# Performance work log

Measured on AMD Instinct MI355X. Metric: run time of the kernel, lower is better.

Reference implementation:

```python
import jax, jax.numpy as jnp
import numpy as np

N = 100000
E = 1600000
D = 128


def setup_inputs() -> dict:
    key = jax.random.key(0)
    k1, k2, k3 = jax.random.split(key, 3)
    indices = jax.random.randint(k1, (2, E), 0, N, dtype=jnp.int64)
    values = jax.random.normal(k2, (E,), dtype=jnp.float32)
    b = jax.random.normal(k3, (N, D), dtype=jnp.float32)
    return {"indices": indices, "values": values, "n": N, "b": b}


def reference(indices, values, n, b):
    # Sparse COO SpMM: out[r] = sum_{e: row[e]==r} values[e] * b[col[e]]
    row, col = indices[0], indices[1]
    contrib = values[:, None] * b[col]          # [E, D] gather-multiply
    out = jax.ops.segment_sum(contrib, row, num_segments=n)  # [N, D] scatter-add
    return out
```

## Files before the change

### kernel.cpp

```cpp
#include <hip/hip_runtime.h>
#include <hip/hip_fp16.h>


#define D_DIM 128
#define RPB 64
#define RPB_SHIFT 6
#define MAXB 2048
#define CAP_LDS 1408
#define EPT 6
#define EPT1 8
#define OVF_MAX 65536

typedef float fx4 __attribute__((ext_vector_type(4)));

__global__ __launch_bounds__(256) void convert_b_kernel(
        const float* __restrict__ b, __half* __restrict__ bh, int n8) {
    int i = blockIdx.x * blockDim.x + threadIdx.x;
    if (i >= n8) return;
    const float4* b4 = (const float4*)b;
    float4 a0 = b4[2 * i];
    float4 a1 = b4[2 * i + 1];
    union { __half2 h[4]; uint4 u; } pk;
    pk.h[0] = __floats2half2_rn(a0.x, a0.y);
    pk.h[1] = __floats2half2_rn(a0.z, a0.w);
    pk.h[2] = __floats2half2_rn(a1.x, a1.y);
    pk.h[3] = __floats2half2_rn(a1.z, a1.w);
    ((uint4*)bh)[i] = pk.u;
}

__global__ __launch_bounds__(1024) void phase1_partition(
        const int* __restrict__ rows,
        const int* __restrict__ cols,
        const float* __restrict__ vals,
        int* __restrict__ bucket_cnt,
        int2* __restrict__ packed,
        int* __restrict__ ovf_cnt,
        int* __restrict__ ovf_list,
        int E, int nb, int cap, int chunk) {
    __shared__ int hist[MAXB];
    int tid = threadIdx.x;
    int start = blockIdx.x * chunk;
    int end = start + chunk; if (end > E) end = E;

    for (int i = tid; i < nb; i += 1024) hist[i] = 0;
    __syncthreads();

    int rr[EPT1]; int cc[EPT1]; float vv[EPT1];
    int ne = 0;
    for (int e = start + tid; e < end; e += 1024) {
        int r = rows[e];
        if (ne < EPT1) { rr[ne] = r; cc[ne] = cols[e]; vv[ne] = vals[e]; }
        ++ne;
        atomicAdd(&hist[r >> RPB_SHIFT], 1);
    }
    __syncthreads();

    for (int bkt = tid; bkt < nb; bkt += 1024) {
        int c = hist[bkt];
        hist[bkt] = (c > 0) ? atomicAdd(&bucket_cnt[bkt], c) : 0;
    }
    __syncthreads();

    int j = 0;
    for (int e = start + tid; e < end; e += 1024, ++j) {
        int r, c; float v;
        if (j < EPT1) { r = rr[j]; c = cc[j]; v = vv[j]; }
        else          { r = rows[e]; c = cols[e]; v = vals[e]; }
        int bkt = r >> RPB_SHIFT;
        int local = atomicAdd(&hist[bkt], 1);
        if (local < cap) {
            int key = ((r & (RPB - 1)) << 17) | c;
            packed[(size_t)bkt * cap + local] = make_int2(key, __float_as_int(v));
        } else {
            int k = atomicAdd(ovf_cnt, 1);
            if (k < OVF_MAX) ovf_list[k] = e;
        }
    }
}

template <bool HALF>
__global__ __launch_bounds__(256) void phase2_sort_gather(
        const int* __restrict__ bucket_cnt,
        const int2* __restrict__ packed,
        const __half* __restrict__ bh,
        const float* __restrict__ b,
        float* __restrict__ out,
        int cap, int N) {
    __shared__ int2 sorted[CAP_LDS];
    __shared__ int hist[RPB];
    __shared__ int offs[RPB + 1];
    __shared__ int cursor[RPB];

    int bucket = blockIdx.x;
    int tid = threadIdx.x;

    int cnt = bucket_cnt[bucket];
    if (cnt > cap) cnt = cap;
    const int2* pk = packed + (size_t)bucket * cap;

    if (tid < RPB) hist[tid] = 0;
    __syncthreads();

    int2 ev[EPT];
    int  rl[EPT];
    int ne = 0;
    for (int i = tid; i < cnt; i += 256) {
        int2 e = pk[i];
        ev[ne] = e;
        rl[ne] = ((unsigned)e.x) >> 17;
        atomicAdd(&hist[rl[ne]], 1);
        ++ne;
    }
    __syncthreads();

    for (int d = 1; d < RPB; d <<= 1) {
        int t = (tid < RPB && tid >= d) ? hist[tid - d] : 0;
        __syncthreads();
        if (tid < RPB) hist[tid] += t;
        __syncthreads();
    }
    if (tid == 0) offs[0] = 0;
    if (tid < RPB) {
        offs[tid + 1] = hist[tid];
        cursor[tid] = (tid == 0) ? 0 : hist[tid - 1];
    }
    __syncthreads();

    for (int j = 0; j < ne; ++j) {
        int pos = atomicAdd(&cursor[rl[j]], 1);
        sorted[pos] = make_int2(ev[j].x & 0x1FFFF, ev[j].y);
    }
    __syncthreads();

    int g = tid >> 5;
    int glane = tid & 31;
    int r0 = bucket << RPB_SHIFT;
    for (int k = 0; k < 8; ++k) {
        int rr = g * 8 + k;
        int start = offs[rr];
        int num = offs[rr + 1] - start;
        float4 acc = make_float4(0.f, 0.f, 0.f, 0.f);
        for (int base = 0; base < num; base += 8) {
#pragma unroll
            for (int j = 0; j < 8; ++j) {
                int idx = base + j;
                int sidx = start + ((idx < num) ? idx : (num - 1));
                int2 e = sorted[sidx];
                float v = (idx < num) ? __int_as_float(e.y) : 0.f;
                if (HALF) {
                    uint2 hv = ((const uint2*)(bh + (size_t)e.x * D_DIM))[glane];
                    __half2* hp = (__half2*)&hv;
                    float2 f0 = __half22float2(hp[0]);
                    float2 f1 = __half22float2(hp[1]);
                    acc.x += v * f0.x;
                    acc.y += v * f0.y;
                    acc.z += v * f1.x;
                    acc.w += v * f1.y;
                } else {
                    float4 bv = ((const float4*)(b + (size_t)e.x * D_DIM))[glane];
                    acc.x += v * bv.x;
                    acc.y += v * bv.y;
                    acc.z += v * bv.z;
                    acc.w += v * bv.w;
                }
            }
        }
        int r = r0 + rr;
        if (r < N) {
            fx4 av = {acc.x, acc.y, acc.z, acc.w};
            __builtin_nontemporal_store(av, (fx4*)(out + (size_t)r * D_DIM) + glane);
        }
    }
}

__global__ void fixup_kernel(const int* __restrict__ ovf_cnt,
                             const int* __restrict__ ovf_list,
                             const int* __restrict__ rows,
                             const int* __restrict__ cols,
                             const float* __restrict__ vals,
                             const float* __restrict__ b,
                             float* __restrict__ out) {
    int items = *ovf_cnt;
    if (items > OVF_MAX) items = OVF_MAX;
    int gsz  = (gridDim.x * blockDim.x) >> 5;
    int gid  = (blockIdx.x * blockDim.x + threadIdx.x) >> 5;
    int lane = threadIdx.x & 31;
    for (int i = gid; i < items; i += gsz) {
        int e = ovf_list[i];
        int r = rows[e];
        int c = cols[e];
        float v = vals[e];
        float4 bv = ((const float4*)(b + (size_t)c * D_DIM))[lane];
        float* op = out + (size_t)r * D_DIM + (size_t)lane * 4;
        atomicAdd(op + 0, v * bv.x);
        atomicAdd(op + 1, v * bv.y);
        atomicAdd(op + 2, v * bv.z);
        atomicAdd(op + 3, v * bv.w);
    }
}

__global__ void spmm_atomic_kernel(const int* __restrict__ rows,
                                   const int* __restrict__ cols,
                                   const float* __restrict__ vals,
                                   const float* __restrict__ b,
                                   float* __restrict__ out, int E) {
    int t = blockIdx.x * blockDim.x + threadIdx.x;
    int e = t >> 5;
    if (e >= E) return;
    int lane = t & 31;
    int r = rows[e];
    int c = cols[e];
    float v = vals[e];
    float4 bv = ((const float4*)(b + (size_t)c * D_DIM))[lane];
    float* op = out + (size_t)r * D_DIM + (size_t)lane * 4;
    atomicAdd(op + 0, v * bv.x);
    atomicAdd(op + 1, v * bv.y);
    atomicAdd(op + 2, v * bv.z);
    atomicAdd(op + 3, v * bv.w);
}

extern "C" void kernel_launch(void* const* d_in, const int* in_sizes, int n_in,
                              void* d_out, int out_size, void* d_ws, size_t ws_size,
                              hipStream_t stream) {
    const int*   indices = (const int*)d_in[0];
    const float* vals    = (const float*)d_in[1];
    const float* b       = (const float*)d_in[3];
    float*       out     = (float*)d_out;

    int E = in_sizes[1];
    int N = out_size / D_DIM;
    const int* rows = indices;
    const int* cols = indices + E;

    int nb = (N + RPB - 1) >> RPB_SHIFT;
    int avg = (nb > 0) ? E / nb : 0;
    int cap = CAP_LDS;

    size_t fixed      = (size_t)nb * 4 + 4 + (size_t)OVF_MAX * 4;
    size_t bh_off     = (fixed + 255) & ~(size_t)255;
    size_t bh_bytes   = (size_t)N * D_DIM * 2;
    size_t packed_h   = (bh_off + bh_bytes + 255) & ~(size_t)255;
    size_t packed_f   = bh_off;
    size_t need_h     = packed_h + (size_t)nb * cap * 8;
    size_t need_f     = packed_f + (size_t)nb * cap * 8;

    bool okBase = (nb <= MAXB) && (N <= 131072) && (cap > avg + avg / 8);
    bool useHalf = okBase && (ws_size >= need_h);
    bool useF32  = okBase && !useHalf && (ws_size >= need_f);

    if (!useHalf && !useF32) {
        (void)hipMemsetAsync(d_out, 0, (size_t)out_size * sizeof(float), stream);
        long long total = (long long)E * 32;
        int blocks = (int)((total + 255) / 256);
        spmm_atomic_kernel<<<blocks, 256, 0, stream>>>(rows, cols, vals, b, out, E);
        return;
    }

    char* w = (char*)d_ws;
    int*    bucket_cnt = (int*)w;
    int*    ovf_cnt    = (int*)(w + (size_t)nb * 4);
    int*    ovf_list   = (int*)(w + (size_t)nb * 4 + 4);
    __half* bh         = (__half*)(w + bh_off);
    int2*   packed     = (int2*)(w + (useHalf ? packed_h : packed_f));

    (void)hipMemsetAsync(bucket_cnt, 0, (size_t)nb * 4 + 4, stream);

    if (useHalf) {
        int n8 = N * D_DIM / 8;
        convert_b_kernel<<<(n8 + 255) / 256, 256, 0, stream>>>(b, bh, n8);
    }

    const int P1_WGS = 256;
    int chunk = (E + P1_WGS - 1) / P1_WGS;
    phase1_partition<<<P1_WGS, 1024, 0, stream>>>(
        rows, cols, vals, bucket_cnt, packed, ovf_cnt, ovf_list, E, nb, cap, chunk);

    if (useHalf)
        phase2_sort_gather<true><<<nb, 256, 0, stream>>>(
            bucket_cnt, packed, bh, b, out, cap, N);
    else
        phase2_sort_gather<false><<<nb, 256, 0, stream>>>(
            bucket_cnt, packed, bh, b, out, cap, N);

    fixup_kernel<<<8, 256, 0, stream>>>(ovf_cnt, ovf_list, rows, cols, vals, b, out);
}
```

Baseline: 215.3 us.

## Fuse fp16 conversion into partition kernel, pad bucket counters, nontemporal loads

The separate kernel that converts b to fp16 is folded into the partition launch as extra workgroups, so conversion runs alongside partitioning and one launch is saved. Each global bucket counter is now spaced 16 ints apart to cut atomic contention from false sharing on the same cache line. The phase-2 reads of packed entries use nontemporal loads to avoid polluting the cache. The counter padding enlarges the workspace, and the conversion blocks compete with partition blocks for CUs.

```diff
diff --git a/kernel.cpp b/kernel.cpp
--- a/kernel.cpp
+++ b/kernel.cpp
@@ -12,23 +12,9 @@
 #define OVF_MAX 65536
 
 typedef float fx4 __attribute__((ext_vector_type(4)));
-
-__global__ __launch_bounds__(256) void convert_b_kernel(
-        const float* __restrict__ b, __half* __restrict__ bh, int n8) {
-    int i = blockIdx.x * blockDim.x + threadIdx.x;
-    if (i >= n8) return;
-    const float4* b4 = (const float4*)b;
-    float4 a0 = b4[2 * i];
-    float4 a1 = b4[2 * i + 1];
-    union { __half2 h[4]; uint4 u; } pk;
-    pk.h[0] = __floats2half2_rn(a0.x, a0.y);
-    pk.h[1] = __floats2half2_rn(a0.z, a0.w);
-    pk.h[2] = __floats2half2_rn(a1.x, a1.y);
-    pk.h[3] = __floats2half2_rn(a1.z, a1.w);
-    ((uint4*)bh)[i] = pk.u;
-}
-
-__global__ __launch_bounds__(1024) void phase1_partition(
+typedef int   ix2 __attribute__((ext_vector_type(2)));
+
+__global__ __launch_bounds__(1024) void phase1_fused(
         const int* __restrict__ rows,
         const int* __restrict__ cols,
         const float* __restrict__ vals,
@@ -36,9 +22,29 @@
         int2* __restrict__ packed,
         int* __restrict__ ovf_cnt,
         int* __restrict__ ovf_list,
-        int E, int nb, int cap, int chunk) {
+        int E, int nb, int cap, int chunk, int cs,
+        int nPart,
+        const float* __restrict__ b, __half* __restrict__ bh, int n8) {
     __shared__ int hist[MAXB];
     int tid = threadIdx.x;
+
+    if ((int)blockIdx.x >= nPart) {
+        int idx = ((int)blockIdx.x - nPart) * 1024 + tid;
+        int stride = ((int)gridDim.x - nPart) * 1024;
+        const float4* b4 = (const float4*)b;
+        for (int i = idx; i < n8; i += stride) {
+            float4 a0 = b4[2 * i];
+            float4 a1 = b4[2 * i + 1];
+            union { __half2 h[4]; uint4 u; } pk;
+            pk.h[0] = __floats2half2_rn(a0.x, a0.y);
+            pk.h[1] = __floats2half2_rn(a0.z, a0.w);
+            pk.h[2] = __floats2half2_rn(a1.x, a1.y);
+            pk.h[3] = __floats2half2_rn(a1.z, a1.w);
+            ((uint4*)bh)[i] = pk.u;
+        }
+        return;
+    }
+
     int start = blockIdx.x * chunk;
     int end = start + chunk; if (end > E) end = E;
 
@@ -57,7 +63,7 @@
 
     for (int bkt = tid; bkt < nb; bkt += 1024) {
         int c = hist[bkt];
-        hist[bkt] = (c > 0) ? atomicAdd(&bucket_cnt[bkt], c) : 0;
+        hist[bkt] = (c > 0) ? atomicAdd(&bucket_cnt[bkt << cs], c) : 0;
     }
     __syncthreads();
 
@@ -85,7 +91,7 @@
         const __half* __restrict__ bh,
         const float* __restrict__ b,
         float* __restrict__ out,
-        int cap, int N) {
+        int cap, int N, int cs) {
     __shared__ int2 sorted[CAP_LDS];
     __shared__ int hist[RPB];
     __shared__ int offs[RPB + 1];
@@ -94,9 +100,9 @@
     int bucket = blockIdx.x;
     int tid = threadIdx.x;
 
-    int cnt = bucket_cnt[bucket];
+    int cnt = bucket_cnt[bucket << cs];
     if (cnt > cap) cnt = cap;
-    const int2* pk = packed + (size_t)bucket * cap;
+    const ix2* pk = (const ix2*)(packed + (size_t)bucket * cap);
 
     if (tid < RPB) hist[tid] = 0;
     __syncthreads();
@@ -105,7 +111,8 @@
     int  rl[EPT];
     int ne = 0;
     for (int i = tid; i < cnt; i += 256) {
-        int2 e = pk[i];
+        ix2 ee = __builtin_nontemporal_load(&pk[i]);
+        int2 e = make_int2(ee.x, ee.y);
         ev[ne] = e;
         rl[ne] = ((unsigned)e.x) >> 17;
         atomicAdd(&hist[rl[ne]], 1);
@@ -236,17 +243,26 @@
     int avg = (nb > 0) ? E / nb : 0;
     int cap = CAP_LDS;
 
-    size_t fixed      = (size_t)nb * 4 + 4 + (size_t)OVF_MAX * 4;
-    size_t bh_off     = (fixed + 255) & ~(size_t)255;
-    size_t bh_bytes   = (size_t)N * D_DIM * 2;
-    size_t packed_h   = (bh_off + bh_bytes + 255) & ~(size_t)255;
-    size_t packed_f   = bh_off;
-    size_t need_h     = packed_h + (size_t)nb * cap * 8;
-    size_t need_f     = packed_f + (size_t)nb * cap * 8;
-
     bool okBase = (nb <= MAXB) && (N <= 131072) && (cap > avg + avg / 8);
-    bool useHalf = okBase && (ws_size >= need_h);
-    bool useF32  = okBase && !useHalf && (ws_size >= need_f);
+    int cs = 4;
+    bool useHalf = false, useF32 = false;
+    size_t cnt_bytes = 0, bh_off = 0, packed_off = 0;
+    size_t bh_bytes = (size_t)N * D_DIM * 2;
+
+    for (int attempt = 0; attempt < 2 && okBase; ++attempt) {
+        cnt_bytes = ((size_t)nb << cs) * 4;
+        size_t fixed = cnt_bytes + 4 + (size_t)OVF_MAX * 4;
+        size_t bho   = (fixed + 255) & ~(size_t)255;
+        size_t pk_h  = (bho + bh_bytes + 255) & ~(size_t)255;
+        size_t pk_f  = bho;
+        if (ws_size >= pk_h + (size_t)nb * cap * 8) {
+            useHalf = true; bh_off = bho; packed_off = pk_h; break;
+        }
+        if (ws_size >= pk_f + (size_t)nb * cap * 8) {
+            useF32 = true; bh_off = bho; packed_off = pk_f; break;
+        }
+        cs = 0;
+    }
 
     if (!useHalf && !useF32) {
         (void)hipMemsetAsync(d_out, 0, (size_t)out_size * sizeof(float), stream);
@@ -258,29 +274,28 @@
 
     char* w = (char*)d_ws;
     int*    bucket_cnt = (int*)w;
-    int*    ovf_cnt    = (int*)(w + (size_t)nb * 4);
-    int*    ovf_list   = (int*)(w + (size_t)nb * 4 + 4);
+    int*    ovf_cnt    = (int*)(w + cnt_bytes);
+    int*    ovf_list   = (int*)(w + cnt_bytes + 4);
     __half* bh         = (__half*)(w + bh_off);
-    int2*   packed     = (int2*)(w + (useHalf ? packed_h : packed_f));
-
-    (void)hipMemsetAsync(bucket_cnt, 0, (size_t)nb * 4 + 4, stream);
-
-    if (useHalf) {
-        int n8 = N * D_DIM / 8;
-        convert_b_kernel<<<(n8 + 255) / 256, 256, 0, stream>>>(b, bh, n8);
-    }
+    int2*   packed     = (int2*)(w + packed_off);
+
+    (void)hipMemsetAsync(bucket_cnt, 0, cnt_bytes + 4, stream);
 
     const int P1_WGS = 256;
     int chunk = (E + P1_WGS - 1) / P1_WGS;
-    phase1_partition<<<P1_WGS, 1024, 0, stream>>>(
-        rows, cols, vals, bucket_cnt, packed, ovf_cnt, ovf_list, E, nb, cap, chunk);
+    int n8 = N * D_DIM / 8;
+    int nConv = useHalf ? ((n8 + 1024 * 2 - 1) / (1024 * 2)) : 0;
+
+    phase1_fused<<<P1_WGS + nConv, 1024, 0, stream>>>(
+        rows, cols, vals, bucket_cnt, packed, ovf_cnt, ovf_list,
+        E, nb, cap, chunk, cs, P1_WGS, b, bh, n8);
 
     if (useHalf)
         phase2_sort_gather<true><<<nb, 256, 0, stream>>>(
-            bucket_cnt, packed, bh, b, out, cap, N);
+            bucket_cnt, packed, bh, b, out, cap, N, cs);
     else
         phase2_sort_gather<false><<<nb, 256, 0, stream>>>(
-            bucket_cnt, packed, bh, b, out, cap, N);
+            bucket_cnt, packed, bh, b, out, cap, N, cs);
 
     fixup_kernel<<<8, 256, 0, stream>>>(ovf_cnt, ovf_list, rows, cols, vals, b, out);
 }
```

New measurement: 227.1 us. 1.06x slower.

## Split feature dimension into column slices for phase2 gather with sliced half layout

Applied to the files above, without the earlier changes.

Converts b into a slice-major half layout in which each 16-column slice of all rows is stored contiguously. Phase 2 now launches one workgroup per (slice, bucket), with four lanes per row covering that slice, so each slice's gather working set (about 3.2 MB) is small enough to stay in cache. The cost is that every workgroup repeats the bucket load, histogram and LDS sort eight times, and each gathered row piece is only 32 bytes, which may lower memory efficiency.

```diff
diff --git a/kernel.cpp b/kernel.cpp
--- a/kernel.cpp
+++ b/kernel.cpp
@@ -10,22 +10,30 @@
 #define EPT 6
 #define EPT1 8
 #define OVF_MAX 65536
+#define NSLICE 8
+#define SLICE_COLS 16
 
 typedef float fx4 __attribute__((ext_vector_type(4)));
 
-__global__ __launch_bounds__(256) void convert_b_kernel(
-        const float* __restrict__ b, __half* __restrict__ bh, int n8) {
-    int i = blockIdx.x * blockDim.x + threadIdx.x;
-    if (i >= n8) return;
-    const float4* b4 = (const float4*)b;
-    float4 a0 = b4[2 * i];
-    float4 a1 = b4[2 * i + 1];
-    union { __half2 h[4]; uint4 u; } pk;
+__global__ __launch_bounds__(256) void convert_b_slice(
+        const float* __restrict__ b, __half* __restrict__ bh, int N) {
+    int i = blockIdx.x * 256 + threadIdx.x;
+    if (i >= N * NSLICE) return;
+    int row = i >> 3, slice = i & 7;
+    const float4* src = (const float4*)(b + (size_t)row * D_DIM + slice * SLICE_COLS);
+    float4 a0 = src[0], a1 = src[1], a2 = src[2], a3 = src[3];
+    union { __half2 h[8]; uint4 u[2]; } pk;
     pk.h[0] = __floats2half2_rn(a0.x, a0.y);
     pk.h[1] = __floats2half2_rn(a0.z, a0.w);
     pk.h[2] = __floats2half2_rn(a1.x, a1.y);
     pk.h[3] = __floats2half2_rn(a1.z, a1.w);
-    ((uint4*)bh)[i] = pk.u;
+    pk.h[4] = __floats2half2_rn(a2.x, a2.y);
+    pk.h[5] = __floats2half2_rn(a2.z, a2.w);
+    pk.h[6] = __floats2half2_rn(a3.x, a3.y);
+    pk.h[7] = __floats2half2_rn(a3.z, a3.w);
+    uint4* dst = (uint4*)(bh + (size_t)slice * N * SLICE_COLS + (size_t)row * SLICE_COLS);
+    dst[0] = pk.u[0];
+    dst[1] = pk.u[1];
 }
 
 __global__ __launch_bounds__(1024) void phase1_partition(
@@ -79,7 +87,7 @@
 }
 
 template <bool HALF>
-__global__ __launch_bounds__(256) void phase2_sort_gather(
+__global__ __launch_bounds__(256) void phase2_sliced(
         const int* __restrict__ bucket_cnt,
         const int2* __restrict__ packed,
         const __half* __restrict__ bh,
@@ -91,7 +99,8 @@
     __shared__ int offs[RPB + 1];
     __shared__ int cursor[RPB];
 
-    int bucket = blockIdx.x;
+    int bucket = blockIdx.y;
+    int slice  = blockIdx.x;
     int tid = threadIdx.x;
 
     int cnt = bucket_cnt[bucket];
@@ -132,44 +141,43 @@
     }
     __syncthreads();
 
-    int g = tid >> 5;
-    int glane = tid & 31;
-    int r0 = bucket << RPB_SHIFT;
-    for (int k = 0; k < 8; ++k) {
-        int rr = g * 8 + k;
-        int start = offs[rr];
-        int num = offs[rr + 1] - start;
-        float4 acc = make_float4(0.f, 0.f, 0.f, 0.f);
-        for (int base = 0; base < num; base += 8) {
+    int s = tid >> 2;
+    int lane4 = tid & 3;
+    const __half* bs = bh + (size_t)slice * N * SLICE_COLS;
+    int start = offs[s];
+    int num = offs[s + 1] - start;
+    float4 acc = make_float4(0.f, 0.f, 0.f, 0.f);
+    for (int base = 0; base < num; base += 8) {
 #pragma unroll
-            for (int j = 0; j < 8; ++j) {
-                int idx = base + j;
-                int sidx = start + ((idx < num) ? idx : (num - 1));
-                int2 e = sorted[sidx];
-                float v = (idx < num) ? __int_as_float(e.y) : 0.f;
-                if (HALF) {
-                    uint2 hv = ((const uint2*)(bh + (size_t)e.x * D_DIM))[glane];
-                    __half2* hp = (__half2*)&hv;
-                    float2 f0 = __half22float2(hp[0]);
-                    float2 f1 = __half22float2(hp[1]);
-                    acc.x += v * f0.x;
-                    acc.y += v * f0.y;
-                    acc.z += v * f1.x;
-                    acc.w += v * f1.y;
-                } else {
-                    float4 bv = ((const float4*)(b + (size_t)e.x * D_DIM))[glane];
-                    acc.x += v * bv.x;
-                    acc.y += v * bv.y;
-                    acc.z += v * bv.z;
-                    acc.w += v * bv.w;
-                }
+        for (int j = 0; j < 8; ++j) {
+            int idx = base + j;
+            int sidx = start + ((idx < num) ? idx : (num - 1));
+            int2 e = sorted[sidx];
+            float v = (idx < num) ? __int_as_float(e.y) : 0.f;
+            if (HALF) {
+                uint2 hv = ((const uint2*)(bs + (size_t)e.x * SLICE_COLS))[lane4];
+                __half2* hp = (__half2*)&hv;
+                float2 f0 = __half22float2(hp[0]);
+                float2 f1 = __half22float2(hp[1]);
+                acc.x += v * f0.x;
+                acc.y += v * f0.y;
+                acc.z += v * f1.x;
+                acc.w += v * f1.y;
+            } else {
+                float4 bv = ((const float4*)(b + (size_t)e.x * D_DIM
+                                             + slice * SLICE_COLS))[lane4];
+                acc.x += v * bv.x;
+                acc.y += v * bv.y;
+                acc.z += v * bv.z;
+                acc.w += v * bv.w;
             }
         }
-        int r = r0 + rr;
-        if (r < N) {
-            fx4 av = {acc.x, acc.y, acc.z, acc.w};
-            __builtin_nontemporal_store(av, (fx4*)(out + (size_t)r * D_DIM) + glane);
-        }
+    }
+    int r = (bucket << RPB_SHIFT) + s;
+    if (r < N) {
+        fx4 av = {acc.x, acc.y, acc.z, acc.w};
+        __builtin_nontemporal_store(av,
+            (fx4*)(out + (size_t)r * D_DIM + slice * SLICE_COLS) + lane4);
     }
 }
 
@@ -266,8 +274,8 @@
     (void)hipMemsetAsync(bucket_cnt, 0, (size_t)nb * 4 + 4, stream);
 
     if (useHalf) {
-        int n8 = N * D_DIM / 8;
-        convert_b_kernel<<<(n8 + 255) / 256, 256, 0, stream>>>(b, bh, n8);
+        int items = N * NSLICE;
+        convert_b_slice<<<(items + 255) / 256, 256, 0, stream>>>(b, bh, N);
     }
 
     const int P1_WGS = 256;
@@ -275,11 +283,12 @@
     phase1_partition<<<P1_WGS, 1024, 0, stream>>>(
         rows, cols, vals, bucket_cnt, packed, ovf_cnt, ovf_list, E, nb, cap, chunk);
 
+    dim3 g2(NSLICE, nb);
     if (useHalf)
-        phase2_sort_gather<true><<<nb, 256, 0, stream>>>(
+        phase2_sliced<true><<<g2, 256, 0, stream>>>(
             bucket_cnt, packed, bh, b, out, cap, N);
     else
-        phase2_sort_gather<false><<<nb, 256, 0, stream>>>(
+        phase2_sliced<false><<<g2, 256, 0, stream>>>(
             bucket_cnt, packed, bh, b, out, cap, N);
 
     fixup_kernel<<<8, 256, 0, stream>>>(ovf_cnt, ovf_list, rows, cols, vals, b, out);
```

Result: slower. 255.4 us (+18.6%).

## Add per-row fixed-capacity bucketing path with one-row-per-32-lane-group gather

Applied to the files above, without the earlier changes.

Adds a new path that scatters COO entries into fixed-capacity per-row slots via a global atomic counter per row. A second kernel then has each 32-lane group sum one output row from the fp16 copy of b and write it directly. This replaces the 64-row bucket partition plus LDS sort stage, removing the sort and the atomic output accumulation. In exchange it performs a global atomic per edge, leaves slots unused for rows with fewer entries, and sends entries past capacity (up to 40) to the overflow fixup. The path is taken whenever the workspace can hold at least 28 slots per row.

```diff
diff --git a/kernel.cpp b/kernel.cpp
--- a/kernel.cpp
+++ b/kernel.cpp
@@ -10,6 +10,8 @@
 #define EPT 6
 #define EPT1 8
 #define OVF_MAX 65536
+#define CAPR_MIN 28
+#define CAPR_MAX 40
 
 typedef float fx4 __attribute__((ext_vector_type(4)));
 
@@ -27,6 +29,80 @@
     pk.h[3] = __floats2half2_rn(a1.z, a1.w);
     ((uint4*)bh)[i] = pk.u;
 }
+
+
+__global__ __launch_bounds__(256) void phase1_rows(
+        const int* __restrict__ rows,
+        const int* __restrict__ cols,
+        const float* __restrict__ vals,
+        int* __restrict__ row_cnt,
+        int2* __restrict__ packed,
+        int* __restrict__ ovf_cnt,
+        int* __restrict__ ovf_list,
+        int E, int capr) {
+    int idx = blockIdx.x * 256 + threadIdx.x;
+    int stride = gridDim.x * 256;
+    for (int e = idx; e < E; e += stride) {
+        int r = rows[e];
+        int c = cols[e];
+        float v = vals[e];
+        int local = atomicAdd(&row_cnt[r], 1);
+        if (local < capr) {
+            packed[(size_t)r * capr + local] = make_int2(c, __float_as_int(v));
+        } else {
+            int k = atomicAdd(ovf_cnt, 1);
+            if (k < OVF_MAX) ovf_list[k] = e;
+        }
+    }
+}
+
+template <bool HALF>
+__global__ __launch_bounds__(256) void phase2_rows(
+        const int* __restrict__ row_cnt,
+        const int2* __restrict__ packed,
+        const __half* __restrict__ bh,
+        const float* __restrict__ b,
+        float* __restrict__ out,
+        int capr, int N) {
+    int g = threadIdx.x >> 5;
+    int glane = threadIdx.x & 31;
+    int r = blockIdx.x * 8 + g;
+    if (r >= N) return;
+
+    int cnt = row_cnt[r];
+    if (cnt > capr) cnt = capr;
+    const int2* pk = packed + (size_t)r * capr;
+
+    float4 acc = make_float4(0.f, 0.f, 0.f, 0.f);
+    for (int base = 0; base < cnt; base += 8) {
+#pragma unroll
+        for (int j = 0; j < 8; ++j) {
+            int idx = base + j;
+            int sidx = (idx < cnt) ? idx : (cnt - 1);
+            int2 e = pk[sidx];
+            float v = (idx < cnt) ? __int_as_float(e.y) : 0.f;
+            if (HALF) {
+                uint2 hv = ((const uint2*)(bh + (size_t)e.x * D_DIM))[glane];
+                __half2* hp = (__half2*)&hv;
+                float2 f0 = __half22float2(hp[0]);
+                float2 f1 = __half22float2(hp[1]);
+                acc.x += v * f0.x;
+                acc.y += v * f0.y;
+                acc.z += v * f1.x;
+                acc.w += v * f1.y;
+            } else {
+                float4 bv = ((const float4*)(b + (size_t)e.x * D_DIM))[glane];
+                acc.x += v * bv.x;
+                acc.y += v * bv.y;
+                acc.z += v * bv.z;
+                acc.w += v * bv.w;
+            }
+        }
+    }
+    fx4 av = {acc.x, acc.y, acc.z, acc.w};
+    __builtin_nontemporal_store(av, (fx4*)(out + (size_t)r * D_DIM) + glane);
+}
+
 
 __global__ __launch_bounds__(1024) void phase1_partition(
         const int* __restrict__ rows,
@@ -232,13 +308,48 @@
     const int* rows = indices;
     const int* cols = indices + E;
 
+    size_t bh_bytes = (size_t)N * D_DIM * 2;
+    int n8 = N * D_DIM / 8;
+
+    {
+        size_t fixedR = (size_t)N * 4 + 4 + (size_t)OVF_MAX * 4;
+        size_t bh_off = (fixedR + 255) & ~(size_t)255;
+        size_t pk_off = (bh_off + bh_bytes + 255) & ~(size_t)255;
+        size_t avail  = (ws_size > pk_off) ? (ws_size - pk_off) : 0;
+        size_t capr_s = avail / ((size_t)N * 8);
+        int capr = (capr_s > CAPR_MAX) ? CAPR_MAX : (int)capr_s;
+        if (capr >= CAPR_MIN) {
+            char* w = (char*)d_ws;
+            int*    row_cnt  = (int*)w;
+            int*    ovf_cnt  = (int*)(w + (size_t)N * 4);
+            int*    ovf_list = (int*)(w + (size_t)N * 4 + 4);
+            __half* bh       = (__half*)(w + bh_off);
+            int2*   packed   = (int2*)(w + pk_off);
+
+            (void)hipMemsetAsync(row_cnt, 0, (size_t)N * 4 + 4, stream);
+
+            convert_b_kernel<<<(n8 + 255) / 256, 256, 0, stream>>>(b, bh, n8);
+
+            int p1b = 2048;
+            phase1_rows<<<p1b, 256, 0, stream>>>(
+                rows, cols, vals, row_cnt, packed, ovf_cnt, ovf_list, E, capr);
+
+            int p2b = (N + 7) / 8;
+            phase2_rows<true><<<p2b, 256, 0, stream>>>(
+                row_cnt, packed, bh, (const float*)nullptr, out, capr, N);
+
+            fixup_kernel<<<8, 256, 0, stream>>>(
+                ovf_cnt, ovf_list, rows, cols, vals, b, out);
+            return;
+        }
+    }
+
     int nb = (N + RPB - 1) >> RPB_SHIFT;
     int avg = (nb > 0) ? E / nb : 0;
     int cap = CAP_LDS;
 
     size_t fixed      = (size_t)nb * 4 + 4 + (size_t)OVF_MAX * 4;
     size_t bh_off     = (fixed + 255) & ~(size_t)255;
-    size_t bh_bytes   = (size_t)N * D_DIM * 2;
     size_t packed_h   = (bh_off + bh_bytes + 255) & ~(size_t)255;
     size_t packed_f   = bh_off;
     size_t need_h     = packed_h + (size_t)nb * cap * 8;
@@ -265,10 +376,8 @@
 
     (void)hipMemsetAsync(bucket_cnt, 0, (size_t)nb * 4 + 4, stream);
 
-    if (useHalf) {
-        int n8 = N * D_DIM / 8;
+    if (useHalf)
         convert_b_kernel<<<(n8 + 255) / 256, 256, 0, stream>>>(b, bh, n8);
-    }
 
     const int P1_WGS = 256;
     int chunk = (E + P1_WGS - 1) / P1_WGS;
```

After: 294.9 us. +37.0%, slower.
